# Performance work log

Hardware: AMD Instinct MI355X
Metric: run time of the kernel (lower is better)

Reference implementation:

```python
import jax, jax.numpy as jnp
import numpy as np

# Dims: batch, seq, model dim, heads, routes-per-query, bleed-over alpha
B, S, D, H, K_ROUTES = 4, 512, 1024, 16, 64
HD = D // H                      # head_dim = 64
SCALE = 1.0 / float(np.sqrt(HD))
ALPHA = 0.25                     # neighbor bleed-over (forward arg default 0.0; >0 here)
CAUSAL = True
NEG = jnp.float32(-1e9)


def _build_routes(seq_len: int, k: int, depth: int = 8) -> np.ndarray:
    """Cantor-coordinate based positional routes (mirrors _build_positional_routes)."""
    pos = np.arange(seq_len, dtype=np.float64)
    x = pos / max(1, seq_len - 1)
    x = np.clip(x, 1e-6, 1.0 - 1e-6)
    val = np.zeros_like(x)
    factor = 0.5
    for _ in range(depth):
        xs = x * 3.0
        digit = xs.astype(np.int64)
        frac = xs - digit
        val = val + (digit == 2).astype(np.float64) * factor
        x = frac
        factor *= 0.5
    coords = np.clip(val, 0.0, 1.0)
    dist = np.abs(coords[:, None] - coords[None, :])            # [S,S]
    routes = np.argsort(dist, axis=1, kind='stable')[:, :k]     # k smallest distances
    return routes.astype(np.int32)


def setup_inputs() -> dict:
    key = jax.random.key(0)
    k0, k1, k2 = jax.random.split(key, 3)
    x = jax.random.normal(k0, (B, S, D), dtype=jnp.float32)
    # nn.Linear weights stored pre-transposed as [in, out] for clean matmul
    w_qkv = jax.random.normal(k1, (D, 3 * D), dtype=jnp.float32) * (1.0 / np.sqrt(D))
    b_qkv = jnp.zeros((3 * D,), dtype=jnp.float32)
    w_out = jax.random.normal(k2, (D, D), dtype=jnp.float32) * (1.0 / np.sqrt(D))
    b_out = jnp.zeros((D,), dtype=jnp.float32)
    routes = jnp.asarray(_build_routes(S, K_ROUTES), dtype=jnp.int32)  # [S, K]
    return {"x": x, "w_qkv": w_qkv, "b_qkv": b_qkv,
            "w_out": w_out, "b_out": b_out, "routes": routes}


def reference(x, w_qkv, b_qkv, w_out, b_out, routes):
    # QKV projection: [B,S,3D] -> [3,B,H,S,hd]
    qkv = (x @ w_qkv + b_qkv).reshape(B, S, 3, H, HD).transpose(2, 0, 3, 1, 4)
    q, k, v = qkv[0], qkv[1], qkv[2]                 # each [B,H,S,hd]

    r = routes                                        # [S,K]
    k_g = jnp.take(k, r, axis=2)                      # [B,H,S,K,hd]
    v_g = jnp.take(v, r, axis=2)
    if ALPHA > 0.0:
        rl = jnp.clip(r - 1, 0, S - 1)
        rr = jnp.clip(r + 1, 0, S - 1)
        k_g = (1.0 - ALPHA) * k_g + (ALPHA / 2.0) * (jnp.take(k, rl, axis=2) + jnp.take(k, rr, axis=2))
        v_g = (1.0 - ALPHA) * v_g + (ALPHA / 2.0) * (jnp.take(v, rl, axis=2) + jnp.take(v, rr, axis=2))

    scores = jnp.einsum('bhqd,bhqkd->bhqk', q, k_g) * SCALE   # [B,H,S,K]
    if CAUSAL:
        # route index > query position is masked (each query always routes to itself)
        mask = r > jnp.arange(S, dtype=r.dtype)[:, None]       # [S,K]
        scores = jnp.where(mask[None, None], NEG, scores)

    attn = jax.nn.softmax(scores, axis=-1)
    out = jnp.einsum('bhqk,bhqkd->bhqd', attn, v_g)            # [B,H,S,hd]
    out = out.transpose(0, 2, 1, 3).reshape(B, S, D)
    return out @ w_out + b_out
```

## Files before the change

### kernel.cpp

```cpp
#include <hip/hip_runtime.h>
#include <hip/hip_bf16.h>

#define BB 4
#define SS 512
#define DD 1024
#define HH 16
#define KR 64
#define HDIM 64
#define THREE_D 3072
#define M_ROWS 2048
#define SCALE_F 0.125f

typedef __attribute__((ext_vector_type(8))) short short8;
typedef __attribute__((ext_vector_type(4))) float floatx4;

union F8 { short8 s; unsigned int u[4]; unsigned short h[8]; };

__device__ inline float bfu(unsigned short h){ union{unsigned int u; float f;} c; c.u = ((unsigned int)h) << 16; return c.f; }
__device__ inline unsigned short f2bf(float f){
    union{float f; unsigned int u;} c; c.f = f;
    unsigned int u = c.u;
    return (unsigned short)((u + 0x7fffu + ((u >> 16) & 1u)) >> 16);
}

#define GLOAD_LDS16(g, l)                                                     \
    __builtin_amdgcn_global_load_lds(                                         \
        (const __attribute__((address_space(1))) unsigned int*)(g),           \
        (__attribute__((address_space(3))) unsigned int*)(l), 16, 0, 0)

__global__ __launch_bounds__(256) void prep_kernel(
    const float* __restrict__ x, const float* __restrict__ w_qkv,
    const float* __restrict__ w_out, const int* __restrict__ routes,
    unsigned short* __restrict__ xb_sw, unsigned short* __restrict__ wb1_sw,
    unsigned short* __restrict__ wb2_sw, unsigned int* __restrict__ maskg)
{
    const int bx = blockIdx.x;
    const int tid = threadIdx.x;
    if (bx < 1024) {
        int gid = bx * 256 + tid;
        int r  = gid & 127;
        int c  = (gid >> 7) & 3;
        int kt = (gid >> 9) & 31;
        int mt = gid >> 14;
        const float* src = x + ((size_t)(mt * 128 + r)) * 1024 + kt * 32 + c * 8;
        float4 a = *(const float4*)src;
        float4 b = *(const float4*)(src + 4);
        F8 o;
        o.h[0] = f2bf(a.x); o.h[1] = f2bf(a.y); o.h[2] = f2bf(a.z); o.h[3] = f2bf(a.w);
        o.h[4] = f2bf(b.x); o.h[5] = f2bf(b.y); o.h[6] = f2bf(b.z); o.h[7] = f2bf(b.w);
        *(uint4*)(xb_sw + (size_t)gid * 8) = *(uint4*)&o;
    } else if (bx < 3072) {
        const float* w;
        unsigned short* out;
        int gid, N;
        if (bx < 2560) { w = w_qkv; out = wb1_sw; N = THREE_D; gid = (bx - 1024) * 256 + tid; }
        else           { w = w_out; out = wb2_sw; N = DD;      gid = (bx - 2560) * 256 + tid; }
        int r  = gid & 127;
        int c  = (gid >> 7) & 3;
        int kt = (gid >> 9) & 31;
        int nt = gid >> 14;
        int n = nt * 128 + r;
        int kbase = kt * 32 + c * 8;
        F8 o;
#pragma unroll
        for (int j = 0; j < 8; ++j)
            o.h[j] = f2bf(w[(size_t)(kbase + j) * N + n]);
        *(uint4*)(out + (size_t)gid * 8) = *(uint4*)&o;
    } else {
        int q = (bx - 3072) * 256 + tid;
        unsigned int w[16];
#pragma unroll
        for (int i = 0; i < 16; ++i) w[i] = 0u;
        for (int j = 0; j < KR; ++j) {
            int r = routes[q * KR + j];
            if (r <= q) w[r >> 5] |= 1u << (r & 31);
        }
#pragma unroll
        for (int sw = 0; sw < 16; ++sw) maskg[sw * SS + q] = w[sw];
    }
}

__global__ __launch_bounds__(256) void gemm_qkv(
    const unsigned short* __restrict__ Asw,
    const unsigned short* __restrict__ Bsw,
    const float* __restrict__ bias,
    unsigned short* __restrict__ qb, unsigned short* __restrict__ kb,
    unsigned short* __restrict__ vb)
{
    __shared__ __align__(16) unsigned short Sh[17408];
    unsigned short* Alds = Sh;
    unsigned short* Blds = Sh + 8192;

    const int tid  = threadIdx.x;
    const int lane = tid & 63;
    const int wid  = tid >> 6;
    const int l15  = lane & 15;
    const int quad = lane >> 4;
    const int wm   = (wid >> 1) * 64;
    const int wn   = (wid & 1) * 64;

    const unsigned short* Ak = Asw + (size_t)blockIdx.y * 131072;
    const unsigned short* Bk = Bsw + (size_t)blockIdx.x * 131072;

    floatx4 acc[4][4];
#pragma unroll
    for (int i = 0; i < 4; ++i)
#pragma unroll
        for (int j = 0; j < 4; ++j) acc[i][j] = (floatx4){0.f, 0.f, 0.f, 0.f};

    for (int kt2 = 0; kt2 < 16; ++kt2) {
#pragma unroll
        for (int kh = 0; kh < 2; ++kh) {
            const unsigned short* ga = Ak + (kt2 * 2 + kh) * 4096 + wid * 1024 + lane * 8;
            const unsigned short* gb = Bk + (kt2 * 2 + kh) * 4096 + wid * 1024 + lane * 8;
            GLOAD_LDS16(ga,       Alds + kh * 4096 + wid * 1024 + lane * 8);
            GLOAD_LDS16(ga + 512, Alds + kh * 4096 + wid * 1024 + 512 + lane * 8);
            GLOAD_LDS16(gb,       Blds + kh * 4096 + wid * 1024 + lane * 8);
            GLOAD_LDS16(gb + 512, Blds + kh * 4096 + wid * 1024 + 512 + lane * 8);
        }
        __syncthreads();

#pragma unroll
        for (int kh = 0; kh < 2; ++kh) {
            F8 af[4], bf[4];
#pragma unroll
            for (int mi = 0; mi < 4; ++mi)
                af[mi] = *(const F8*)(Alds + kh * 4096 + (size_t)(quad * 128 + wm + mi * 16 + l15) * 8);
#pragma unroll
            for (int ni = 0; ni < 4; ++ni)
                bf[ni] = *(const F8*)(Blds + kh * 4096 + (size_t)(quad * 128 + wn + ni * 16 + l15) * 8);
#pragma unroll
            for (int mi = 0; mi < 4; ++mi)
#pragma unroll
                for (int ni = 0; ni < 4; ++ni)
                    acc[mi][ni] = __builtin_amdgcn_mfma_f32_16x16x32_bf16(
                        af[mi].s, bf[ni].s, acc[mi][ni], 0, 0, 0);
        }
        __syncthreads();
    }

    const int m0 = blockIdx.y * 128;
    const int n0 = blockIdx.x * 128;

#pragma unroll
    for (int mi = 0; mi < 4; ++mi) {
#pragma unroll
        for (int ni = 0; ni < 4; ++ni) {
            int col = wn + ni * 16 + l15;
            float bv = bias[n0 + col];
#pragma unroll
            for (int r = 0; r < 4; ++r) {
                int row = wm + mi * 16 + quad * 4 + r;
                Sh[row * 136 + col] = f2bf(acc[mi][ni][r] + bv);
            }
        }
    }
    __syncthreads();

    for (int i = tid; i < 2048; i += 256) {
        int rr = i >> 4, cc = i & 15;
        int grow = m0 + rr, gcol = n0 + cc * 8;
        int b = grow >> 9, s = grow & 511;
        int which = gcol >> 10, rem = gcol & 1023;
        int h = rem >> 6, hd = rem & 63;
        unsigned short* dst = (which == 0) ? qb : (which == 1) ? kb : vb;
        uint4 val = *(const uint4*)(Sh + rr * 136 + cc * 8);
        *(uint4*)(dst + (((size_t)(b * HH + h) * SS) + s) * HDIM + hd) = val;
    }
}

__global__ __launch_bounds__(256) void gemm_out(
    const unsigned short* __restrict__ Asw,
    const unsigned short* __restrict__ Bsw,
    const float* __restrict__ bias,
    float* __restrict__ Cout)
{
    __shared__ __align__(16) unsigned short Alds[4096];
    __shared__ __align__(16) unsigned short Blds[8192];

    const int tid  = threadIdx.x;
    const int lane = tid & 63;
    const int wid  = tid >> 6;
    const int l15  = lane & 15;
    const int quad = lane >> 4;
    const int mt64 = blockIdx.y;
    const int mt   = mt64 >> 1;
    const int rh   = (mt64 & 1) * 64;
    const int nt   = blockIdx.x;
    const int wn   = wid * 32;

    floatx4 acc[4][2];
#pragma unroll
    for (int i = 0; i < 4; ++i)
#pragma unroll
        for (int j = 0; j < 2; ++j) acc[i][j] = (floatx4){0.f, 0.f, 0.f, 0.f};

    for (int kt2 = 0; kt2 < 16; ++kt2) {
#pragma unroll
        for (int kh = 0; kh < 2; ++kh) {
            int kt = kt2 * 2 + kh;
            const unsigned short* ga = Asw + ((size_t)(mt * 32 + kt) * 4 + wid) * 1024 + (rh + lane) * 8;
            const unsigned short* gb = Bsw + (size_t)(nt * 32 + kt) * 4096 + wid * 1024 + lane * 8;
            GLOAD_LDS16(ga,       Alds + kh * 2048 + wid * 512 + lane * 8);
            GLOAD_LDS16(gb,       Blds + kh * 4096 + wid * 1024 + lane * 8);
            GLOAD_LDS16(gb + 512, Blds + kh * 4096 + wid * 1024 + 512 + lane * 8);
        }
        __syncthreads();

#pragma unroll
        for (int kh = 0; kh < 2; ++kh) {
            F8 af[4], bf[2];
#pragma unroll
            for (int mi = 0; mi < 4; ++mi)
                af[mi] = *(const F8*)(Alds + kh * 2048 + (size_t)(quad * 64 + mi * 16 + l15) * 8);
#pragma unroll
            for (int ni = 0; ni < 2; ++ni)
                bf[ni] = *(const F8*)(Blds + kh * 4096 + (size_t)(quad * 128 + wn + ni * 16 + l15) * 8);
#pragma unroll
            for (int mi = 0; mi < 4; ++mi)
#pragma unroll
                for (int ni = 0; ni < 2; ++ni)
                    acc[mi][ni] = __builtin_amdgcn_mfma_f32_16x16x32_bf16(
                        af[mi].s, bf[ni].s, acc[mi][ni], 0, 0, 0);
        }
        __syncthreads();
    }

    const int m0 = mt64 * 64;
    const int n0 = nt * 128;
#pragma unroll
    for (int mi = 0; mi < 4; ++mi) {
#pragma unroll
        for (int ni = 0; ni < 2; ++ni) {
            int col = n0 + wn + ni * 16 + l15;
            float bv = bias[col];
#pragma unroll
            for (int r = 0; r < 4; ++r) {
                int row = m0 + mi * 16 + quad * 4 + r;
                Cout[(size_t)row * DD + col] = acc[mi][ni][r] + bv;
            }
        }
    }
}

__global__ __launch_bounds__(256) void blend_v_kernel(
    const unsigned short* __restrict__ vb, unsigned short* __restrict__ Vtg)
{
    __shared__ float vt[130][65];
    const int bh = blockIdx.x >> 2;
    const int sb = (blockIdx.x & 3) * 128;
    const int tid = threadIdx.x;
    const unsigned short* vbase = vb + (size_t)bh * SS * HDIM;

    for (int i = tid; i < 130 * 8; i += 256) {
        int row = i >> 3, c8 = (i & 7) << 3;
        int s = sb + row - 1; s = s < 0 ? 0 : (s > SS - 1 ? SS - 1 : s);
        F8 vv = *(const F8*)(vbase + (size_t)s * 64 + c8);
#pragma unroll
        for (int j = 0; j < 8; ++j) vt[row][c8 + j] = bfu(vv.h[j]);
    }
    __syncthreads();

    for (int i = tid; i < 64 * 32; i += 256) {
        int d = i >> 5, s4 = (i & 31) << 2;
        ushort4 o;
        o.x = f2bf(0.75f * vt[s4+1][d] + 0.125f * (vt[s4+0][d] + vt[s4+2][d]));
        o.y = f2bf(0.75f * vt[s4+2][d] + 0.125f * (vt[s4+1][d] + vt[s4+3][d]));
        o.z = f2bf(0.75f * vt[s4+3][d] + 0.125f * (vt[s4+2][d] + vt[s4+4][d]));
        o.w = f2bf(0.75f * vt[s4+4][d] + 0.125f * (vt[s4+3][d] + vt[s4+5][d]));
        *(ushort4*)(Vtg + ((size_t)bh * 64 + d) * SS + sb + s4) = o;
    }
}

__global__ __launch_bounds__(512, 2) void attn_kernel(
    const unsigned short* __restrict__ qb,
    const unsigned short* __restrict__ kbuf,
    const unsigned short* __restrict__ Vtg,
    const unsigned int* __restrict__ maskg,
    unsigned short* __restrict__ attn_sw)
{
    __shared__ __align__(16) unsigned short Ks[512 * 64];
    __shared__ __align__(16) unsigned short Vs[64 * 512];
    __shared__ __align__(16) unsigned short Ps[8 * 16 * 64];

    const int bh = blockIdx.x >> 2;
    const int qt = blockIdx.x & 3;
    const int b = bh >> 4, h = bh & 15;
    const int tid  = threadIdx.x;
    const int lane = tid & 63;
    const int wid  = tid >> 6;
    const int l15  = lane & 15;
    const int quad = lane >> 4;

    {
        const unsigned short* kbh = kbuf + (size_t)bh * (SS * 64);
        uint4* dst = (uint4*)Ks;
        for (int c = tid; c < 4096; c += 512) {
            int s = c >> 3, cc = c & 7;
            int sm = s ? s - 1 : 0;
            int sp = (s < SS - 1) ? s + 1 : SS - 1;
            F8 k0 = *(const F8*)(kbh + (size_t)s  * 64 + cc * 8);
            F8 km = *(const F8*)(kbh + (size_t)sm * 64 + cc * 8);
            F8 kp = *(const F8*)(kbh + (size_t)sp * 64 + cc * 8);
            F8 o;
#pragma unroll
            for (int j = 0; j < 8; ++j)
                o.h[j] = f2bf(0.75f * bfu(k0.h[j]) + 0.125f * (bfu(km.h[j]) + bfu(kp.h[j])));
            dst[(s << 3) | (cc ^ (s & 7))] = *(uint4*)&o;
        }
        const uint4* srcv = (const uint4*)(Vtg + (size_t)bh * (64 * SS));
        uint4* dstv = (uint4*)Vs;
        for (int c = tid; c < 4096; c += 512) {
            int d = c >> 6, sc = c & 63;
            dstv[(d << 6) | (sc & 56) | ((sc ^ d) & 7)] = srcv[c];
        }
    }
    __syncthreads();

    const int qbase = qt * 128 + wid * 16;
    const int q = qbase + l15;

    F8 qf[2];
    {
        const unsigned short* qrow = qb + ((size_t)bh * SS + q) * 64;
        qf[0] = *(const F8*)(qrow + quad * 8);
        qf[1] = *(const F8*)(qrow + 32 + quad * 8);
    }

    floatx4 accS[32];
#pragma unroll
    for (int st = 0; st < 32; ++st) {
        int srow = st * 16 + l15;
        const F8 k0 = *(const F8*)(Ks + (((srow << 3) | ( quad      ^ (srow & 7))) << 3));
        const F8 k1 = *(const F8*)(Ks + (((srow << 3) | ((4 + quad) ^ (srow & 7))) << 3));
        floatx4 a = (floatx4){0.f, 0.f, 0.f, 0.f};
        a = __builtin_amdgcn_mfma_f32_16x16x32_bf16(k0.s, qf[0].s, a, 0, 0, 0);
        a = __builtin_amdgcn_mfma_f32_16x16x32_bf16(k1.s, qf[1].s, a, 0, 0, 0);
        accS[st] = a;
    }

    float m = -1e30f;
    unsigned int mw = 0;
#pragma unroll
    for (int st = 0; st < 32; ++st) {
        if ((st & 1) == 0) mw = maskg[(st >> 1) * SS + q];
        int sbase = (st & 1) * 16 + quad * 4;
        floatx4 a = accS[st];
#pragma unroll
        for (int r = 0; r < 4; ++r) {
            float v = ((mw >> (sbase + r)) & 1u) ? a[r] * SCALE_F : -1e30f;
            a[r] = v;
            m = fmaxf(m, v);
        }
        accS[st] = a;
    }
    m = fmaxf(m, __shfl_xor(m, 16));
    m = fmaxf(m, __shfl_xor(m, 32));

    floatx4 accO[4];
#pragma unroll
    for (int dt = 0; dt < 4; ++dt) accO[dt] = (floatx4){0.f, 0.f, 0.f, 0.f};
    float lsum = 0.f;
    unsigned int* Pw = (unsigned int*)Ps + wid * 512;

#pragma unroll
    for (int ch = 0; ch < 8; ++ch) {
#pragma unroll
        for (int t = 0; t < 4; ++t) {
            floatx4 a = accS[ch * 4 + t];
            float e0 = __expf(a[0] - m), e1 = __expf(a[1] - m);
            float e2 = __expf(a[2] - m), e3 = __expf(a[3] - m);
            lsum += (e0 + e1) + (e2 + e3);
            unsigned int w0 = (unsigned int)f2bf(e0) | ((unsigned int)f2bf(e1) << 16);
            unsigned int w1 = (unsigned int)f2bf(e2) | ((unsigned int)f2bf(e3) << 16);
            int off0 = t * 8 + quad * 2;
            int off1 = off0 + 1;
            Pw[l15 * 32 + ((((off0 >> 2) ^ (l15 & 7)) << 2) | (off0 & 3))] = w0;
            Pw[l15 * 32 + ((((off1 >> 2) ^ (l15 & 7)) << 2) | (off1 & 3))] = w1;
        }
        F8 pa[2];
#pragma unroll
        for (int ks = 0; ks < 2; ++ks) {
            int ci = ks * 4 + quad;
            pa[ks] = *(const F8*)((const unsigned short*)(Pw + l15 * 32) +
                                  ((ci ^ (l15 & 7)) << 3));
        }
#pragma unroll
        for (int dt = 0; dt < 4; ++dt) {
            int d = dt * 16 + l15;
#pragma unroll
            for (int ks = 0; ks < 2; ++ks) {
                int sc = ch * 8 + ks * 4 + quad;
                const F8 bv = *(const F8*)(Vs + (((d << 6) | (sc & 56) | ((sc ^ d) & 7)) << 3));
                accO[dt] = __builtin_amdgcn_mfma_f32_16x16x32_bf16(pa[ks].s, bv.s, accO[dt], 0, 0, 0);
            }
        }
    }

    lsum += __shfl_xor(lsum, 16);
    lsum += __shfl_xor(lsum, 32);
    float inv = 1.0f / lsum;

    unsigned short* Ow = Ps + wid * 1024;
#pragma unroll
    for (int r = 0; r < 4; ++r) {
        float invr = __shfl(inv, quad * 4 + r);
#pragma unroll
        for (int dt = 0; dt < 4; ++dt)
            Ow[(quad * 4 + r) * 64 + dt * 16 + l15] = f2bf(accO[dt][r] * invr);
    }
#pragma unroll
    for (int i = 0; i < 2; ++i) {
        int ch = i * 64 + lane;
        int qlocal = ch >> 3, j = ch & 7;
        int qq = qt * 128 + wid * 16 + qlocal;
        int mrow = b * SS + qq;
        int mt = mrow >> 7, rr = mrow & 127;
        int kt2 = h * 2 + (j >> 2), c = j & 3;
        size_t gid = (((size_t)(mt * 32 + kt2) * 4 + c) * 128 + rr);
        *(uint4*)(attn_sw + gid * 8) = *(const uint4*)(Ow + qlocal * 64 + j * 8);
    }
}

extern "C" void kernel_launch(void* const* d_in, const int* in_sizes, int n_in,
                              void* d_out, int out_size, void* d_ws, size_t ws_size,
                              hipStream_t stream)
{
    const float* x     = (const float*)d_in[0];
    const float* w_qkv = (const float*)d_in[1];
    const float* b_qkv = (const float*)d_in[2];
    const float* w_out = (const float*)d_in[3];
    const float* b_out = (const float*)d_in[4];
    const int* routes  = (const int*)d_in[5];

    char* w = (char*)d_ws;
    unsigned short* xb_sw  = (unsigned short*)(w);
    unsigned short* wb1_sw = (unsigned short*)(w + (4u  << 20));
    unsigned short* wb2_sw = (unsigned short*)(w + (10u << 20));
    unsigned short* qbuf   = (unsigned short*)(w + (12u << 20));
    unsigned short* kbuf   = (unsigned short*)(w + (16u << 20));
    unsigned short* vbuf   = (unsigned short*)(w + (20u << 20));
    unsigned short* Vtg    = (unsigned short*)(w + (24u << 20));
    unsigned short* attnsw = (unsigned short*)(w + (28u << 20));
    unsigned int*   maskg  = (unsigned int*)(w + (32u << 20));

    prep_kernel<<<3074, 256, 0, stream>>>(x, w_qkv, w_out, routes,
                                          xb_sw, wb1_sw, wb2_sw, maskg);

    gemm_qkv<<<dim3(THREE_D / 128, M_ROWS / 128), 256, 0, stream>>>(
        xb_sw, wb1_sw, b_qkv, qbuf, kbuf, vbuf);

    blend_v_kernel<<<256, 256, 0, stream>>>(vbuf, Vtg);

    attn_kernel<<<256, 512, 0, stream>>>(qbuf, kbuf, Vtg, maskg, attnsw);

    gemm_out<<<dim3(DD / 128, M_ROWS / 64), 256, 0, stream>>>(
        attnsw, wb2_sw, b_out, (float*)d_out);
}
```

Before: 151.4 us.

## Fuse V blend/transpose into attention kernel and drop softmax max pass

```diff
diff --git a/kernel.cpp b/kernel.cpp
--- a/kernel.cpp
+++ b/kernel.cpp
@@ -243,39 +243,10 @@
     }
 }
 
-__global__ __launch_bounds__(256) void blend_v_kernel(
-    const unsigned short* __restrict__ vb, unsigned short* __restrict__ Vtg)
-{
-    __shared__ float vt[130][65];
-    const int bh = blockIdx.x >> 2;
-    const int sb = (blockIdx.x & 3) * 128;
-    const int tid = threadIdx.x;
-    const unsigned short* vbase = vb + (size_t)bh * SS * HDIM;
-
-    for (int i = tid; i < 130 * 8; i += 256) {
-        int row = i >> 3, c8 = (i & 7) << 3;
-        int s = sb + row - 1; s = s < 0 ? 0 : (s > SS - 1 ? SS - 1 : s);
-        F8 vv = *(const F8*)(vbase + (size_t)s * 64 + c8);
-#pragma unroll
-        for (int j = 0; j < 8; ++j) vt[row][c8 + j] = bfu(vv.h[j]);
-    }
-    __syncthreads();
-
-    for (int i = tid; i < 64 * 32; i += 256) {
-        int d = i >> 5, s4 = (i & 31) << 2;
-        ushort4 o;
-        o.x = f2bf(0.75f * vt[s4+1][d] + 0.125f * (vt[s4+0][d] + vt[s4+2][d]));
-        o.y = f2bf(0.75f * vt[s4+2][d] + 0.125f * (vt[s4+1][d] + vt[s4+3][d]));
-        o.z = f2bf(0.75f * vt[s4+3][d] + 0.125f * (vt[s4+2][d] + vt[s4+4][d]));
-        o.w = f2bf(0.75f * vt[s4+4][d] + 0.125f * (vt[s4+3][d] + vt[s4+5][d]));
-        *(ushort4*)(Vtg + ((size_t)bh * 64 + d) * SS + sb + s4) = o;
-    }
-}
-
 __global__ __launch_bounds__(512, 2) void attn_kernel(
     const unsigned short* __restrict__ qb,
     const unsigned short* __restrict__ kbuf,
-    const unsigned short* __restrict__ Vtg,
+    const unsigned short* __restrict__ vbuf,
     const unsigned int* __restrict__ maskg,
     unsigned short* __restrict__ attn_sw)
 {
@@ -308,11 +279,26 @@
                 o.h[j] = f2bf(0.75f * bfu(k0.h[j]) + 0.125f * (bfu(km.h[j]) + bfu(kp.h[j])));
             dst[(s << 3) | (cc ^ (s & 7))] = *(uint4*)&o;
         }
-        const uint4* srcv = (const uint4*)(Vtg + (size_t)bh * (64 * SS));
-        uint4* dstv = (uint4*)Vs;
-        for (int c = tid; c < 4096; c += 512) {
-            int d = c >> 6, sc = c & 63;
-            dstv[(d << 6) | (sc & 56) | ((sc ^ d) & 7)] = srcv[c];
+        const unsigned short* vbh = vbuf + (size_t)bh * (SS * 64);
+        const int a8 = tid & 7;
+        const int cc = (tid >> 3) & 7;
+        const int s0 = ((tid >> 6) << 3) + a8;
+#pragma unroll
+        for (int k = 0; k < 8; ++k) {
+            int s = s0 + k * 64;
+            int sm = s ? s - 1 : 0;
+            int sp = (s < SS - 1) ? s + 1 : SS - 1;
+            F8 v0 = *(const F8*)(vbh + (size_t)s  * 64 + cc * 8);
+            F8 vm = *(const F8*)(vbh + (size_t)sm * 64 + cc * 8);
+            F8 vp = *(const F8*)(vbh + (size_t)sp * 64 + cc * 8);
+            int sc = s >> 3;
+#pragma unroll
+            for (int j = 0; j < 8; ++j) {
+                int d = cc * 8 + j;
+                float bv = 0.75f * bfu(v0.h[j]) + 0.125f * (bfu(vm.h[j]) + bfu(vp.h[j]));
+                int chunk = (d << 6) | (sc & 56) | ((sc ^ d ^ cc) & 7);
+                Vs[(chunk << 3) | (s & 7)] = f2bf(bv);
+            }
         }
     }
     __syncthreads();
@@ -339,24 +325,6 @@
         accS[st] = a;
     }
 
-    float m = -1e30f;
-    unsigned int mw = 0;
-#pragma unroll
-    for (int st = 0; st < 32; ++st) {
-        if ((st & 1) == 0) mw = maskg[(st >> 1) * SS + q];
-        int sbase = (st & 1) * 16 + quad * 4;
-        floatx4 a = accS[st];
-#pragma unroll
-        for (int r = 0; r < 4; ++r) {
-            float v = ((mw >> (sbase + r)) & 1u) ? a[r] * SCALE_F : -1e30f;
-            a[r] = v;
-            m = fmaxf(m, v);
-        }
-        accS[st] = a;
-    }
-    m = fmaxf(m, __shfl_xor(m, 16));
-    m = fmaxf(m, __shfl_xor(m, 32));
-
     floatx4 accO[4];
 #pragma unroll
     for (int dt = 0; dt < 4; ++dt) accO[dt] = (floatx4){0.f, 0.f, 0.f, 0.f};
@@ -365,11 +333,17 @@
 
 #pragma unroll
     for (int ch = 0; ch < 8; ++ch) {
+        unsigned int mw0 = maskg[(ch * 2) * SS + q];
+        unsigned int mw1 = maskg[(ch * 2 + 1) * SS + q];
 #pragma unroll
         for (int t = 0; t < 4; ++t) {
+            unsigned int mw = (t & 2) ? mw1 : mw0;
+            int sbase = (t & 1) * 16 + quad * 4;
             floatx4 a = accS[ch * 4 + t];
-            float e0 = __expf(a[0] - m), e1 = __expf(a[1] - m);
-            float e2 = __expf(a[2] - m), e3 = __expf(a[3] - m);
+            float e0 = ((mw >> (sbase + 0)) & 1u) ? __expf(a[0] * SCALE_F) : 0.f;
+            float e1 = ((mw >> (sbase + 1)) & 1u) ? __expf(a[1] * SCALE_F) : 0.f;
+            float e2 = ((mw >> (sbase + 2)) & 1u) ? __expf(a[2] * SCALE_F) : 0.f;
+            float e3 = ((mw >> (sbase + 3)) & 1u) ? __expf(a[3] * SCALE_F) : 0.f;
             lsum += (e0 + e1) + (e2 + e3);
             unsigned int w0 = (unsigned int)f2bf(e0) | ((unsigned int)f2bf(e1) << 16);
             unsigned int w1 = (unsigned int)f2bf(e2) | ((unsigned int)f2bf(e3) << 16);
@@ -391,7 +365,8 @@
 #pragma unroll
             for (int ks = 0; ks < 2; ++ks) {
                 int sc = ch * 8 + ks * 4 + quad;
-                const F8 bv = *(const F8*)(Vs + (((d << 6) | (sc & 56) | ((sc ^ d) & 7)) << 3));
+                int chunk = (d << 6) | (sc & 56) | ((sc ^ d ^ (d >> 3)) & 7);
+                const F8 bv = *(const F8*)(Vs + (chunk << 3));
                 accO[dt] = __builtin_amdgcn_mfma_f32_16x16x32_bf16(pa[ks].s, bv.s, accO[dt], 0, 0, 0);
             }
         }
@@ -440,9 +415,8 @@
     unsigned short* qbuf   = (unsigned short*)(w + (12u << 20));
     unsigned short* kbuf   = (unsigned short*)(w + (16u << 20));
     unsigned short* vbuf   = (unsigned short*)(w + (20u << 20));
-    unsigned short* Vtg    = (unsigned short*)(w + (24u << 20));
-    unsigned short* attnsw = (unsigned short*)(w + (28u << 20));
-    unsigned int*   maskg  = (unsigned int*)(w + (32u << 20));
+    unsigned short* attnsw = (unsigned short*)(w + (24u << 20));
+    unsigned int*   maskg  = (unsigned int*)(w + (28u << 20));
 
     prep_kernel<<<3074, 256, 0, stream>>>(x, w_qkv, w_out, routes,
                                           xb_sw, wb1_sw, wb2_sw, maskg);
@@ -450,9 +424,7 @@
     gemm_qkv<<<dim3(THREE_D / 128, M_ROWS / 128), 256, 0, stream>>>(
         xb_sw, wb1_sw, b_qkv, qbuf, kbuf, vbuf);
 
-    blend_v_kernel<<<256, 256, 0, stream>>>(vbuf, Vtg);
-
-    attn_kernel<<<256, 512, 0, stream>>>(qbuf, kbuf, Vtg, maskg, attnsw);
+    attn_kernel<<<256, 512, 0, stream>>>(qbuf, kbuf, vbuf, maskg, attnsw);
 
     gemm_out<<<dim3(DD / 128, M_ROWS / 64), 256, 0, stream>>>(
         attnsw, wb2_sw, b_out, (float*)d_out);
```

Result: slower. 162.1 us (+7.1%).
